# Optimization experiments

Measured on AMD Instinct MI355X. Metric: run time of the kernel, lower is better.

The kernel has to match this reference:

```python
import jax, jax.numpy as jnp
import numpy as np

N_NODES = 100000
N_EDGES = 1600000
N_GRAPHS = 256
F_IN = 38
HID = 64


def graph_conv(x, edge_index, w_rel, b_rel, w_root):
    # PyG GraphConv (aggr='add'): out = lin_rel(sum_{j in N(i)} x_j) + lin_root(x_i)
    src, dst = edge_index[0], edge_index[1]
    agg = jax.ops.segment_sum(x[src], dst, num_segments=N_NODES)  # [N, F]
    return agg @ w_rel + b_rel + x @ w_root


def setup_inputs() -> dict:
    key = jax.random.key(0)
    ks = jax.random.split(key, 10)
    x = jax.random.normal(ks[0], (N_NODES, F_IN), dtype=jnp.float32)
    edge_index = jax.random.randint(ks[1], (2, N_EDGES), 0, N_NODES, dtype=jnp.int64)
    batch = jnp.sort(jax.random.randint(ks[2], (N_NODES,), 0, N_GRAPHS, dtype=jnp.int64))
    s1 = 1.0 / np.sqrt(F_IN)
    s2 = 1.0 / np.sqrt(HID)
    w1_rel = jax.random.uniform(ks[3], (F_IN, HID), jnp.float32, -s1, s1)
    b1_rel = jax.random.uniform(ks[4], (HID,), jnp.float32, -s1, s1)
    w1_root = jax.random.uniform(ks[5], (F_IN, HID), jnp.float32, -s1, s1)
    w2_rel = jax.random.uniform(ks[6], (HID, HID), jnp.float32, -s2, s2)
    b2_rel = jax.random.uniform(ks[7], (HID,), jnp.float32, -s2, s2)
    w2_root = jax.random.uniform(ks[8], (HID, HID), jnp.float32, -s2, s2)
    return {"x": x, "edge_index": edge_index, "batch": batch,
            "w1_rel": w1_rel, "b1_rel": b1_rel, "w1_root": w1_root,
            "w2_rel": w2_rel, "b2_rel": b2_rel, "w2_root": w2_root}


def reference(x, edge_index, batch, w1_rel, b1_rel, w1_root, w2_rel, b2_rel, w2_root):
    h = graph_conv(x, edge_index, w1_rel, b1_rel, w1_root)
    h = jax.nn.relu(h)
    h = graph_conv(h, edge_index, w2_rel, b2_rel, w2_root)
    # global_mean_pool: segment mean over batch ids
    sums = jax.ops.segment_sum(h, batch, num_segments=N_GRAPHS)  # [G, HID]
    counts = jax.ops.segment_sum(jnp.ones((N_NODES,), h.dtype), batch, num_segments=N_GRAPHS)
    pooled = sums / jnp.maximum(counts, 1.0)[:, None]
    # dropout(p=0.5, training=False) is identity in eval mode
    return jax.nn.relu(pooled)
```

## Files before the change

kernel.cpp:

```cpp
#include <hip/hip_runtime.h>

#define N_NODES 100000
#define N_EDGES 1600000
#define N_GRAPHS 256
#define F_IN 38
#define F_PAD 40
#define HID 64
#define CAPD 48

#define NB   391
#define EPB  4096
#define NBLK 391
#define BCAP 4608

typedef unsigned short ushort;
typedef unsigned int uint;
typedef _Float16 h2 __attribute__((ext_vector_type(2)));

__device__ __forceinline__ h2 u2h(uint u) {
    union { uint u; h2 h; } v; v.u = u; return v.h;
}
__device__ __forceinline__ uint h2u(h2 h) {
    union { uint u; h2 h; } v; v.h = h; return v.u;
}
__device__ __forceinline__ ushort f2h_bits(float f) {
    union { _Float16 h; ushort s; } v; v.h = (_Float16)f; return v.s;
}
__device__ __forceinline__ int clampi(int v) {
    return (int)min((uint)v, (uint)N_NODES);
}

__global__ void pack_x_kernel(const float* __restrict__ x,
                              ushort* __restrict__ xb,
                              ushort* __restrict__ hb) {
    int tid = blockIdx.x * blockDim.x + threadIdx.x;
    if (tid < HID) hb[(N_NODES << 6) + tid] = 0;
    if (tid >= (N_NODES + 1) * F_PAD) return;
    int n = tid / F_PAD;
    int f = tid - n * F_PAD;
    float v = (n < N_NODES && f < F_IN) ? x[n * F_IN + f] : 0.0f;
    xb[tid] = f2h_bits(v);
}

__global__ void scatter_kernel(const int* __restrict__ src,
                               const int* __restrict__ dst,
                               int* __restrict__ gcur,
                               uint* __restrict__ ebuf) {
    __shared__ int hist[NB];
    __shared__ int cur[NB];
    for (int i = threadIdx.x; i < NB; i += 256) hist[i] = 0;
    __syncthreads();
    const int base = blockIdx.x * EPB;
    int d[EPB / 256];
    uint pl[EPB / 256];
    #pragma unroll
    for (int i = 0; i < EPB / 256; ++i) {
        int e = base + i * 256 + threadIdx.x;
        d[i] = (e < N_EDGES) ? dst[e] : -1;
        if (d[i] >= 0) {
            pl[i] = ((uint)src[e] << 8) | ((uint)d[i] & 255u);
            atomicAdd(&hist[d[i] >> 8], 1);
        }
    }
    __syncthreads();
    for (int i = threadIdx.x; i < NB; i += 256) {
        int c = hist[i];
        cur[i] = (c > 0) ? atomicAdd(&gcur[i], c) : 0;
    }
    __syncthreads();
    #pragma unroll
    for (int i = 0; i < EPB / 256; ++i) {
        if (d[i] >= 0) {
            int b = d[i] >> 8;
            int pos = atomicAdd(&cur[b], 1);
            if (pos < BCAP) ebuf[b * BCAP + pos] = pl[i];
        }
    }
}

__global__ __launch_bounds__(256, 3) void build_kernel(
        const uint* __restrict__ ebuf,
        const int* __restrict__ gcur,
        int* __restrict__ cnt,
        int* __restrict__ slots) {
    __shared__ int cl[256];
    __shared__ int s_slots[256 * CAPD];
    const int b = blockIdx.x;
    cl[threadIdx.x] = 0;
    for (int i = threadIdx.x; i < 256 * CAPD; i += 256) s_slots[i] = N_NODES;
    __syncthreads();
    int e1 = gcur[b]; if (e1 > BCAP) e1 = BCAP;
    for (int idx = threadIdx.x; idx < e1; idx += 256) {
        uint e = ebuf[b * BCAP + idx];
        int dl = (int)(e & 255u);
        int pos = atomicAdd(&cl[dl], 1);
        if (pos < CAPD) s_slots[dl * CAPD + pos] = (int)(e >> 8);
    }
    __syncthreads();
    int n = (b << 8) + threadIdx.x;
    if (n < N_NODES) cnt[n] = cl[threadIdx.x];
    int nrows = N_NODES - (b << 8);
    if (nrows > 256) nrows = 256;
    int lim = nrows * (CAPD / 4);
    const int4* sp = (const int4*)s_slots;
    int4* gp = (int4*)(slots + b * 256 * CAPD);
    for (int i = threadIdx.x; i < lim; i += 256) gp[i] = sp[i];
}

__global__ __launch_bounds__(256, 4) void layer1_kernel(
        const uint* __restrict__ xb32,
        const int* __restrict__ cnt,
        const int* __restrict__ slots,
        const float* __restrict__ w_rel,
        const float* __restrict__ b_rel,
        const float* __restrict__ w_root,
        const int* __restrict__ batch,
        ushort* __restrict__ hb,
        float* __restrict__ hsum) {
    __shared__ uint s_wrelp[20 * HID];
    __shared__ uint s_wrootp[20 * HID];
    __shared__ uint s_a[64][20];
    __shared__ uint s_x[64][20];
    for (int i = threadIdx.x; i < 20 * HID; i += 256) {
        int kk = i >> 6, cc = i & 63;
        int k0 = 2 * kk, k1 = 2 * kk + 1;
        float r0 = (k0 < F_IN) ? w_rel[k0 * HID + cc] : 0.f;
        float r1 = (k1 < F_IN) ? w_rel[k1 * HID + cc] : 0.f;
        float o0 = (k0 < F_IN) ? w_root[k0 * HID + cc] : 0.f;
        float o1 = (k1 < F_IN) ? w_root[k1 * HID + cc] : 0.f;
        s_wrelp[i]  = (uint)f2h_bits(r0) | ((uint)f2h_bits(r1) << 16);
        s_wrootp[i] = (uint)f2h_bits(o0) | ((uint)f2h_bits(o1) << 16);
    }
    const int wave = threadIdx.x >> 6, lane = threadIdx.x & 63;
    const int half = lane >> 5, l32 = lane & 31;
    const int base = blockIdx.x * 64;

    for (int i = 0; i < 8; ++i) {
        int nl = wave * 16 + 2 * i + half;
        int n = base + nl;
        uint xv = 0;
        int dp = 0;
        if (n < N_NODES) {
            int deg = cnt[n]; if (deg > CAPD) deg = CAPD;
            dp = (deg + 15) & ~15; if (dp > CAPD) dp = CAPD;
            if (l32 < 20) xv = xb32[n * 20 + l32];
        }
        h2 sum = {(_Float16)0, (_Float16)0};
        const int* sl = slots + n * CAPD;
        for (int j = 0; j < dp; j += 16) {
            int4 a4 = *(const int4*)(sl + j);
            int4 b4 = *(const int4*)(sl + j + 4);
            int4 c4 = *(const int4*)(sl + j + 8);
            int4 d4 = *(const int4*)(sl + j + 12);
            if (l32 < 20) {
                uint v0 = xb32[clampi(a4.x) * 20 + l32];
                uint v1 = xb32[clampi(a4.y) * 20 + l32];
                uint v2 = xb32[clampi(a4.z) * 20 + l32];
                uint v3 = xb32[clampi(a4.w) * 20 + l32];
                uint v4 = xb32[clampi(b4.x) * 20 + l32];
                uint v5 = xb32[clampi(b4.y) * 20 + l32];
                uint v6 = xb32[clampi(b4.z) * 20 + l32];
                uint v7 = xb32[clampi(b4.w) * 20 + l32];
                uint v8 = xb32[clampi(c4.x) * 20 + l32];
                uint v9 = xb32[clampi(c4.y) * 20 + l32];
                uint va = xb32[clampi(c4.z) * 20 + l32];
                uint vb = xb32[clampi(c4.w) * 20 + l32];
                uint vc = xb32[clampi(d4.x) * 20 + l32];
                uint vd = xb32[clampi(d4.y) * 20 + l32];
                uint ve = xb32[clampi(d4.z) * 20 + l32];
                uint vf = xb32[clampi(d4.w) * 20 + l32];
                h2 t0 = (u2h(v0) + u2h(v1)) + (u2h(v2) + u2h(v3));
                h2 t1 = (u2h(v4) + u2h(v5)) + (u2h(v6) + u2h(v7));
                h2 t2 = (u2h(v8) + u2h(v9)) + (u2h(va) + u2h(vb));
                h2 t3 = (u2h(vc) + u2h(vd)) + (u2h(ve) + u2h(vf));
                sum += (t0 + t1) + (t2 + t3);
            }
        }
        if (l32 < 20) {
            s_a[nl][l32] = h2u(sum);
            s_x[nl][l32] = xv;
        }
    }
    __syncthreads();

    const int c = lane, r = wave;
    const float bias = b_rel[c];
    float psum = 0.f;
    int cur_g = -1;
    for (int i = 0; i < 16; ++i) {
        int nl = r * 16 + i;
        int n = base + nl;
        if (n >= N_NODES) break;
        h2 acc = {(_Float16)0, (_Float16)0};
        #pragma unroll
        for (int k8 = 0; k8 < 5; ++k8) {
            uint4 pa = *(const uint4*)&s_a[nl][k8 * 4];
            uint4 px = *(const uint4*)&s_x[nl][k8 * 4];
            acc += u2h(pa.x) * u2h(s_wrelp[(k8 * 4 + 0) * HID + c]);
            acc += u2h(pa.y) * u2h(s_wrelp[(k8 * 4 + 1) * HID + c]);
            acc += u2h(pa.z) * u2h(s_wrelp[(k8 * 4 + 2) * HID + c]);
            acc += u2h(pa.w) * u2h(s_wrelp[(k8 * 4 + 3) * HID + c]);
            acc += u2h(px.x) * u2h(s_wrootp[(k8 * 4 + 0) * HID + c]);
            acc += u2h(px.y) * u2h(s_wrootp[(k8 * 4 + 1) * HID + c]);
            acc += u2h(px.z) * u2h(s_wrootp[(k8 * 4 + 2) * HID + c]);
            acc += u2h(px.w) * u2h(s_wrootp[(k8 * 4 + 3) * HID + c]);
        }
        float hv = fmaxf((float)acc.x + (float)acc.y + bias, 0.f);
        hb[(n << 6) + c] = f2h_bits(hv);
        int g = batch[n];
        if (g != cur_g) {
            if (cur_g >= 0) atomicAdd(&hsum[(cur_g << 6) + c], psum);
            psum = 0.f;
            cur_g = g;
        }
        psum += hv;
    }
    if (cur_g >= 0) atomicAdd(&hsum[(cur_g << 6) + c], psum);
}

__global__ __launch_bounds__(256, 8) void layer2_kernel(
        const uint* __restrict__ hb32,
        const int* __restrict__ cnt,
        const int* __restrict__ slots,
        const int* __restrict__ batch,
        float* __restrict__ esum) {
    const int wave = threadIdx.x >> 6, lane = threadIdx.x & 63;
    const int half = lane >> 5, l32 = lane & 31;
    const int base = blockIdx.x * 64;

    float psum0 = 0.f, psum1 = 0.f;
    int cur_g = -1;
    for (int i = 0; i < 8; ++i) {
        int n = base + wave * 16 + 2 * i + half;
        if (n < N_NODES) {
            int deg = cnt[n]; if (deg > CAPD) deg = CAPD;
            int dp = (deg + 15) & ~15; if (dp > CAPD) dp = CAPD;
            h2 sum = {(_Float16)0, (_Float16)0};
            const int* sl = slots + n * CAPD;
            for (int j = 0; j < dp; j += 16) {
                int4 a4 = *(const int4*)(sl + j);
                int4 b4 = *(const int4*)(sl + j + 4);
                int4 c4 = *(const int4*)(sl + j + 8);
                int4 d4 = *(const int4*)(sl + j + 12);
                uint v0 = hb32[(clampi(a4.x) << 5) + l32];
                uint v1 = hb32[(clampi(a4.y) << 5) + l32];
                uint v2 = hb32[(clampi(a4.z) << 5) + l32];
                uint v3 = hb32[(clampi(a4.w) << 5) + l32];
                uint v4 = hb32[(clampi(b4.x) << 5) + l32];
                uint v5 = hb32[(clampi(b4.y) << 5) + l32];
                uint v6 = hb32[(clampi(b4.z) << 5) + l32];
                uint v7 = hb32[(clampi(b4.w) << 5) + l32];
                uint v8 = hb32[(clampi(c4.x) << 5) + l32];
                uint v9 = hb32[(clampi(c4.y) << 5) + l32];
                uint va = hb32[(clampi(c4.z) << 5) + l32];
                uint vb = hb32[(clampi(c4.w) << 5) + l32];
                uint vc = hb32[(clampi(d4.x) << 5) + l32];
                uint vd = hb32[(clampi(d4.y) << 5) + l32];
                uint ve = hb32[(clampi(d4.z) << 5) + l32];
                uint vf = hb32[(clampi(d4.w) << 5) + l32];
                h2 t0 = (u2h(v0) + u2h(v1)) + (u2h(v2) + u2h(v3));
                h2 t1 = (u2h(v4) + u2h(v5)) + (u2h(v6) + u2h(v7));
                h2 t2 = (u2h(v8) + u2h(v9)) + (u2h(va) + u2h(vb));
                h2 t3 = (u2h(vc) + u2h(vd)) + (u2h(ve) + u2h(vf));
                sum += (t0 + t1) + (t2 + t3);
            }
            int g = batch[n];
            if (g != cur_g) {
                if (cur_g >= 0) {
                    atomicAdd(&esum[(cur_g << 6) + 2 * l32], psum0);
                    atomicAdd(&esum[(cur_g << 6) + 2 * l32 + 1], psum1);
                }
                psum0 = 0.f; psum1 = 0.f;
                cur_g = g;
            }
            psum0 += (float)sum.x;
            psum1 += (float)sum.y;
        }
    }
    if (cur_g >= 0) {
        atomicAdd(&esum[(cur_g << 6) + 2 * l32], psum0);
        atomicAdd(&esum[(cur_g << 6) + 2 * l32 + 1], psum1);
    }
}

__global__ void finalize_kernel(const float* __restrict__ esum,
                                const float* __restrict__ hsum,
                                const float* __restrict__ w2_rel,
                                const float* __restrict__ w2_root,
                                const float* __restrict__ b2,
                                const int* __restrict__ batch,
                                float* __restrict__ out) {
    __shared__ float s_e[HID];
    __shared__ float s_h[HID];
    const int g = blockIdx.x;
    const int c = threadIdx.x;
    s_e[c] = esum[(g << 6) + c];
    s_h[c] = hsum[(g << 6) + c];
    __syncthreads();

    int lo = 0, hi = N_NODES;
    while (lo < hi) { int m = (lo + hi) >> 1; if (batch[m] < g) lo = m + 1; else hi = m; }
    int start = lo;
    hi = N_NODES;
    while (lo < hi) { int m = (lo + hi) >> 1; if (batch[m] < g + 1) lo = m + 1; else hi = m; }
    int cntg = lo - start;

    float acc = (float)cntg * b2[c];
    #pragma unroll
    for (int k = 0; k < HID; ++k) {
        acc += s_e[k] * w2_rel[k * HID + c];
        acc += s_h[k] * w2_root[k * HID + c];
    }
    float denom = cntg > 0 ? (float)cntg : 1.f;
    out[(g << 6) + c] = fmaxf(acc / denom, 0.f);
}

extern "C" void kernel_launch(void* const* d_in, const int* in_sizes, int n_in,
                              void* d_out, int out_size, void* d_ws, size_t ws_size,
                              hipStream_t stream) {
    const float* x       = (const float*)d_in[0];
    const int*   ei      = (const int*)  d_in[1];
    const int*   batch   = (const int*)  d_in[2];
    const float* w1_rel  = (const float*)d_in[3];
    const float* b1_rel  = (const float*)d_in[4];
    const float* w1_root = (const float*)d_in[5];
    const float* w2_rel  = (const float*)d_in[6];
    const float* b2_rel  = (const float*)d_in[7];
    const float* w2_root = (const float*)d_in[8];
    float* out = (float*)d_out;

    const int* src = ei;
    const int* dst = ei + N_EDGES;

    char* wsb = (char*)d_ws;
    int*    cnt   = (int*)   (wsb);
    float*  hsum  = (float*) (wsb + 400000);
    float*  esum  = (float*) (wsb + 465536);
    int*    gcur  = (int*)   (wsb + 531072);
    int*    slots = (int*)   (wsb + 532640);
    ushort* xb    = (ushort*)(wsb + 19732640);
    ushort* hb    = (ushort*)(wsb + 27732720);
    uint*   ebuf  = (uint*)  (wsb + 19732640);

    hipMemsetAsync(wsb + 400000, 0, 132636, stream);

    scatter_kernel<<<NBLK, 256, 0, stream>>>(src, dst, gcur, ebuf);
    build_kernel<<<NB, 256, 0, stream>>>(ebuf, gcur, cnt, slots);

    {
        int total = (N_NODES + 1) * F_PAD;
        pack_x_kernel<<<(total + 255) / 256, 256, 0, stream>>>(x, xb, hb);
    }
    {
        int blocks = (N_NODES + 63) / 64;
        layer1_kernel<<<blocks, 256, 0, stream>>>((const uint*)xb, cnt, slots,
                                                  w1_rel, b1_rel, w1_root, batch,
                                                  hb, hsum);
    }
    {
        int blocks = (N_NODES + 63) / 64;
        layer2_kernel<<<blocks, 256, 0, stream>>>((const uint*)hb, cnt, slots,
                                                  batch, esum);
    }
    {
        finalize_kernel<<<N_GRAPHS, HID, 0, stream>>>(esum, hsum, w2_rel, w2_root,
                                                      b2_rel, batch, out);
    }
}
```

Before: 250.3 us.

## Fuse edge scatter with x packing and stage bucketed edges in shared memory

The edge-bucketing scatter and the fp16 packing of x now run in one launch, with extra blocks doing the packing. To allow this, the edge buffer moves into the hb region so it no longer overlaps xb. In the scatter part, each block prefix-scans its bucket histogram and sorts its edges by bucket in shared memory. It then writes them to the global buckets in contiguous runs instead of scattered single writes. The cost is about 30KB of LDS per block, extra syncthreads for the scan, and a more complex kernel that shares launch bounds with the simple packing blocks.

```diff
diff --git a/kernel.cpp b/kernel.cpp
--- a/kernel.cpp
+++ b/kernel.cpp
@@ -10,7 +10,8 @@
 
 #define NB   391
 #define EPB  4096
-#define NBLK 391
+#define EDGE_BLOCKS 391
+#define PACK_BLOCKS 15626
 #define BCAP 4608
 
 typedef unsigned short ushort;
@@ -30,51 +31,91 @@
     return (int)min((uint)v, (uint)N_NODES);
 }
 
-__global__ void pack_x_kernel(const float* __restrict__ x,
-                              ushort* __restrict__ xb,
-                              ushort* __restrict__ hb) {
-    int tid = blockIdx.x * blockDim.x + threadIdx.x;
-    if (tid < HID) hb[(N_NODES << 6) + tid] = 0;
-    if (tid >= (N_NODES + 1) * F_PAD) return;
-    int n = tid / F_PAD;
-    int f = tid - n * F_PAD;
-    float v = (n < N_NODES && f < F_IN) ? x[n * F_IN + f] : 0.0f;
-    xb[tid] = f2h_bits(v);
-}
-
-__global__ void scatter_kernel(const int* __restrict__ src,
-                               const int* __restrict__ dst,
-                               int* __restrict__ gcur,
-                               uint* __restrict__ ebuf) {
-    __shared__ int hist[NB];
-    __shared__ int cur[NB];
+__global__ __launch_bounds__(256, 4) void pre_kernel(
+        const float* __restrict__ x,
+        const int* __restrict__ src,
+        const int* __restrict__ dst,
+        int* __restrict__ gcur,
+        uint* __restrict__ ebuf,
+        ushort* __restrict__ xb,
+        ushort* __restrict__ hb) {
+    __shared__ int    hist[NB];
+    __shared__ int    offs[NB];
+    __shared__ int    cur[NB];
+    __shared__ int    gbase[NB];
+    __shared__ int    scan[512];
+    __shared__ uint   sbuf[EPB];
+    __shared__ ushort sb[EPB];
+
+    const int blk = blockIdx.x;
+    if (blk >= EDGE_BLOCKS) {
+        int tid = (blk - EDGE_BLOCKS) * 256 + threadIdx.x;
+        if (tid < HID) hb[(N_NODES << 6) + tid] = 0;
+        if (tid >= (N_NODES + 1) * F_PAD) return;
+        int n = tid / F_PAD;
+        int f = tid - n * F_PAD;
+        float v = (n < N_NODES && f < F_IN) ? x[n * F_IN + f] : 0.0f;
+        xb[tid] = f2h_bits(v);
+        return;
+    }
+
     for (int i = threadIdx.x; i < NB; i += 256) hist[i] = 0;
     __syncthreads();
-    const int base = blockIdx.x * EPB;
-    int d[EPB / 256];
+
+    const int base = blk * EPB + threadIdx.x;
+    int  bkt[EPB / 256];
     uint pl[EPB / 256];
     #pragma unroll
     for (int i = 0; i < EPB / 256; ++i) {
-        int e = base + i * 256 + threadIdx.x;
-        d[i] = (e < N_EDGES) ? dst[e] : -1;
-        if (d[i] >= 0) {
-            pl[i] = ((uint)src[e] << 8) | ((uint)d[i] & 255u);
-            atomicAdd(&hist[d[i] >> 8], 1);
-        }
-    }
-    __syncthreads();
+        int e = base + i * 256;
+        bkt[i] = -1;
+        if (e < N_EDGES) {
+            int d = dst[e];
+            bkt[i] = d >> 8;
+            pl[i] = ((uint)src[e] << 8) | ((uint)d & 255u);
+            atomicAdd(&hist[bkt[i]], 1);
+        }
+    }
+    __syncthreads();
+
+    {
+        int i0 = threadIdx.x, i1 = threadIdx.x + 256;
+        scan[i0] = (i0 < NB) ? hist[i0] : 0;
+        scan[i1] = (i1 < NB) ? hist[i1] : 0;
+        __syncthreads();
+        for (int d = 1; d < 512; d <<= 1) {
+            int v0 = (i0 >= d) ? scan[i0 - d] : 0;
+            int v1 = (i1 >= d) ? scan[i1 - d] : 0;
+            __syncthreads();
+            scan[i0] += v0;
+            scan[i1] += v1;
+            __syncthreads();
+        }
+    }
     for (int i = threadIdx.x; i < NB; i += 256) {
-        int c = hist[i];
-        cur[i] = (c > 0) ? atomicAdd(&gcur[i], c) : 0;
-    }
-    __syncthreads();
+        int h = hist[i];
+        int o = scan[i] - h;
+        offs[i] = o;
+        cur[i] = o;
+        gbase[i] = (h > 0) ? atomicAdd(&gcur[i], h) : 0;
+    }
+    __syncthreads();
+
     #pragma unroll
     for (int i = 0; i < EPB / 256; ++i) {
-        if (d[i] >= 0) {
-            int b = d[i] >> 8;
-            int pos = atomicAdd(&cur[b], 1);
-            if (pos < BCAP) ebuf[b * BCAP + pos] = pl[i];
-        }
+        if (bkt[i] >= 0) {
+            int pos = atomicAdd(&cur[bkt[i]], 1);
+            sbuf[pos] = pl[i];
+            sb[pos] = (ushort)bkt[i];
+        }
+    }
+    __syncthreads();
+
+    int total = scan[NB - 1];
+    for (int i = threadIdx.x; i < total; i += 256) {
+        int b = sb[i];
+        int p = gbase[b] + (i - offs[b]);
+        if (p < BCAP) ebuf[b * BCAP + p] = sbuf[i];
     }
 }
 
@@ -340,17 +381,16 @@
     int*    slots = (int*)   (wsb + 532640);
     ushort* xb    = (ushort*)(wsb + 19732640);
     ushort* hb    = (ushort*)(wsb + 27732720);
-    uint*   ebuf  = (uint*)  (wsb + 19732640);
+    uint*   ebuf  = (uint*)  (wsb + 27732720);
 
     hipMemsetAsync(wsb + 400000, 0, 132636, stream);
 
-    scatter_kernel<<<NBLK, 256, 0, stream>>>(src, dst, gcur, ebuf);
+    {
+        pre_kernel<<<EDGE_BLOCKS + PACK_BLOCKS, 256, 0, stream>>>(
+            x, src, dst, gcur, ebuf, xb, hb);
+    }
     build_kernel<<<NB, 256, 0, stream>>>(ebuf, gcur, cnt, slots);
 
-    {
-        int total = (N_NODES + 1) * F_PAD;
-        pack_x_kernel<<<(total + 255) / 256, 256, 0, stream>>>(x, xb, hb);
-    }
     {
         int blocks = (N_NODES + 63) / 64;
         layer1_kernel<<<blocks, 256, 0, stream>>>((const uint*)xb, cnt, slots,
```

New measurement: 243.0 us. 2.9% less time.
